# Kernel tuning notes

Measured on AMD Instinct MI355X. Metric: run time of the kernel, lower is better.

The kernel has to match this reference:

```python
import jax, jax.numpy as jnp
import numpy as np

N_NODES = 50000
N_EDGES = 150000
NODE_F, EDGE_F = 4, 11
HID, HID_OUT = 512, 1024
VS, AS_, N_ACT = 2048, 2048, 1000


def _graph_conv(x, W, b, src, dst, n, edge_weight=None):
    # DGL GraphConv, norm='both': D_out^{-1/2} on src feats, sum-aggregate, D_in^{-1/2} on dst.
    deg_out = jnp.maximum(jnp.zeros((n,), x.dtype).at[src].add(1.0), 1.0)
    deg_in = jnp.maximum(jnp.zeros((n,), x.dtype).at[dst].add(1.0), 1.0)
    h = x * (deg_out[:, None] ** -0.5)
    mult_first = W.shape[0] > W.shape[1]
    if mult_first:
        h = h @ W
    m = h[src]  # [E, d] gather
    if edge_weight is not None:
        m = m * edge_weight  # elementwise u_mul_e
    agg = jax.ops.segment_sum(m, dst, num_segments=n)
    if not mult_first:
        agg = agg @ W
    return agg * (deg_in[:, None] ** -0.5) + b


def setup_inputs() -> dict:
    key = jax.random.key(0)
    ks = jax.random.split(key, 16)
    s = 0.05
    return {
        'node_feats': jax.random.normal(ks[0], (N_NODES, NODE_F), jnp.float32),
        'edge_feats': jax.random.normal(ks[1], (N_EDGES, EDGE_F), jnp.float32),
        'W1': jax.random.normal(ks[2], (NODE_F, EDGE_F), jnp.float32) * s,
        'b1': jnp.zeros((EDGE_F,), jnp.float32),
        'W2': jax.random.normal(ks[3], (EDGE_F, HID), jnp.float32) * s,
        'b2': jnp.zeros((HID,), jnp.float32),
        'W3': jax.random.normal(ks[4], (HID, HID_OUT), jnp.float32) * s,
        'b3': jnp.zeros((HID_OUT,), jnp.float32),
        'Wv1': jax.random.normal(ks[5], (HID_OUT, VS), jnp.float32) * s,
        'bv1': jnp.zeros((VS,), jnp.float32),
        'Wv2': jax.random.normal(ks[6], (VS, 1), jnp.float32) * s,
        'bv2': jnp.zeros((1,), jnp.float32),
        'Wa1': jax.random.normal(ks[7], (HID_OUT, AS_), jnp.float32) * s,
        'ba1': jnp.zeros((AS_,), jnp.float32),
        'Wa2': jax.random.normal(ks[8], (AS_, N_ACT), jnp.float32) * s,
        'ba2': jnp.zeros((N_ACT,), jnp.float32),
        'src': jax.random.randint(ks[9], (N_EDGES,), 0, N_NODES, jnp.int32),
        'dst': jax.random.randint(ks[10], (N_EDGES,), 0, N_NODES, jnp.int32),
    }


def reference(node_feats, edge_feats, W1, b1, W2, b2, W3, b3,
              Wv1, bv1, Wv2, bv2, Wa1, ba1, Wa2, ba2, src, dst):
    n = node_feats.shape[0]
    loop = jnp.arange(n, dtype=src.dtype)
    srcL = jnp.concatenate([src, loop])  # add_self_loop
    dstL = jnp.concatenate([dst, loop])
    # self-loop edges get zero edge features (DGL default)
    ef = jnp.concatenate([edge_feats, jnp.zeros((n, edge_feats.shape[1]), edge_feats.dtype)], axis=0)

    h = jax.nn.relu(_graph_conv(node_feats, W1, b1, srcL, dstL, n))          # [N, 11]
    h = jax.nn.relu(_graph_conv(h, W2, b2, srcL, dstL, n, edge_weight=ef))   # [N, 512]
    h = _graph_conv(h, W3, b3, srcL, dstL, n)                                # [N, 1024]

    g_emb = jnp.mean(h, axis=0, keepdims=True)  # dgl.mean_nodes, single graph -> [1, 1024]

    v = jax.nn.relu(g_emb @ Wv1 + bv1) @ Wv2 + bv2        # [1, 1]
    a = jax.nn.relu(g_emb @ Wa1 + ba1) @ Wa2 + ba2        # [1, N_ACT]
    return v + (a - a.mean())
```

## Files before the change

### kernel.cpp

```cpp
#include <hip/hip_runtime.h>

#define NN 50000
#define NE 150000
#define NB 196

__global__ __launch_bounds__(256) void k_deg(const int* __restrict__ src,
                                             const int* __restrict__ dst,
                                             int* __restrict__ deg_out,
                                             int* __restrict__ deg_in) {
    int e = blockIdx.x * 256 + threadIdx.x;
    if (e < NE) {
        atomicAdd(&deg_out[src[e]], 1);
        atomicAdd(&deg_in[dst[e]], 1);
    }
}

__global__ __launch_bounds__(256) void k_bsum(const int* __restrict__ deg_in,
                                              const int* __restrict__ deg_out,
                                              int* __restrict__ bsum_in,
                                              int* __restrict__ bsum_out) {
    __shared__ int si[256], so[256];
    int t = threadIdx.x;
    int idx = blockIdx.x * 256 + t;
    si[t] = (idx < NN) ? deg_in[idx] : 0;
    so[t] = (idx < NN) ? deg_out[idx] : 0;
    __syncthreads();
    for (int off = 128; off >= 1; off >>= 1) {
        if (t < off) { si[t] += si[t + off]; so[t] += so[t + off]; }
        __syncthreads();
    }
    if (t == 0) { bsum_in[blockIdx.x] = si[0]; bsum_out[blockIdx.x] = so[0]; }
}

__global__ __launch_bounds__(256) void k_rowptr(const int* __restrict__ deg_in,
                                                const int* __restrict__ deg_out,
                                                const int* __restrict__ bsum_in,
                                                const int* __restrict__ bsum_out,
                                                const float* __restrict__ x,
                                                int* __restrict__ rp_in,
                                                int* __restrict__ rp_out,
                                                float* __restrict__ dins,
                                                float* __restrict__ douts,
                                                float4* __restrict__ xs4) {
    __shared__ int si[256], so[256];
    int b = blockIdx.x, t = threadIdx.x;
    si[t] = (t < b) ? bsum_in[t] : 0;
    so[t] = (t < b) ? bsum_out[t] : 0;
    __syncthreads();
    for (int off = 128; off >= 1; off >>= 1) {
        if (t < off) { si[t] += si[t + off]; so[t] += so[t + off]; }
        __syncthreads();
    }
    int off_in = si[0], off_out = so[0];
    __syncthreads();
    int idx = b * 256 + t;
    int di = (idx < NN) ? deg_in[idx] : 0;
    int dq = (idx < NN) ? deg_out[idx] : 0;
    si[t] = di; so[t] = dq;
    __syncthreads();
    for (int off = 1; off < 256; off <<= 1) {
        int a = (t >= off) ? si[t - off] : 0;
        int c2 = (t >= off) ? so[t - off] : 0;
        __syncthreads();
        si[t] += a; so[t] += c2;
        __syncthreads();
    }
    if (idx < NN) {
        rp_in[idx]  = off_in  + si[t] - di;
        rp_out[idx] = off_out + so[t] - dq;
        float dif = rsqrtf((float)(di + 1));
        float dqf = rsqrtf((float)(dq + 1));
        dins[idx] = dif;
        douts[idx] = dqf;
        float4 x4 = ((const float4*)x)[idx];
        x4.x *= dqf; x4.y *= dqf; x4.z *= dqf; x4.w *= dqf;
        xs4[idx] = x4;
    }
    if (b == 0 && t == 0) { rp_in[NN] = NE; rp_out[NN] = NE; }
}

__global__ __launch_bounds__(256) void k_scatter(const int* __restrict__ src,
                                                 const int* __restrict__ dst,
                                                 const float* __restrict__ ef,
                                                 const int* __restrict__ rp_in,
                                                 const int* __restrict__ rp_out,
                                                 int* __restrict__ cur_in,
                                                 int* __restrict__ cur_out,
                                                 int* __restrict__ nbr_in,
                                                 float4* __restrict__ ef4,
                                                 int* __restrict__ nbr_out) {
    int e = blockIdx.x * 256 + threadIdx.x;
    if (e >= NE) return;
    int s = src[e], d = dst[e];
    int pi = rp_in[d] + atomicAdd(&cur_in[d], 1);
    nbr_in[pi] = s;
    const float* er = ef + (size_t)e * 11;
    ef4[(size_t)pi * 3 + 0] = make_float4(er[0], er[1], er[2], er[3]);
    ef4[(size_t)pi * 3 + 1] = make_float4(er[4], er[5], er[6], er[7]);
    ef4[(size_t)pi * 3 + 2] = make_float4(er[8], er[9], er[10], 0.f);
    int po = rp_out[s] + atomicAdd(&cur_out[s], 1);
    nbr_out[po] = d;
}

__global__ __launch_bounds__(256) void k_conv1g(const float4* __restrict__ xs4,
                                                const int* __restrict__ nbr_in,
                                                const int* __restrict__ rp_in,
                                                const int* __restrict__ nbr_out,
                                                const int* __restrict__ rp_out,
                                                const float* __restrict__ dins,
                                                const float* __restrict__ douts,
                                                const float* __restrict__ W1,
                                                const float* __restrict__ b1,
                                                float4* __restrict__ h1s4,
                                                float* __restrict__ c) {
    int n = blockIdx.x * 256 + threadIdx.x;
    if (n >= NN) return;
    float din  = dins[n];
    float dout = douts[n];
    float4 a = xs4[n];
    int beg = rp_in[n], end = rp_in[n + 1];
    for (int p = beg; p < end; p++) {
        float4 xs = xs4[nbr_in[p]];
        a.x += xs.x; a.y += xs.y; a.z += xs.z; a.w += xs.w;
    }
    float cacc = din;
    int ob = rp_out[n], oe = rp_out[n + 1];
    for (int p = ob; p < oe; p++)
        cacc += dins[nbr_out[p]];
    c[n] = cacc;
    float y[12];
    #pragma unroll
    for (int j = 0; j < 11; j++) {
        float t2 = a.x * W1[0 * 11 + j] + a.y * W1[1 * 11 + j] +
                   a.z * W1[2 * 11 + j] + a.w * W1[3 * 11 + j];
        y[j] = fmaxf(fmaf(t2, din, b1[j]), 0.f) * dout;
    }
    y[11] = 0.f;
    h1s4[(size_t)n * 3 + 0] = make_float4(y[0], y[1], y[2],  y[3]);
    h1s4[(size_t)n * 3 + 1] = make_float4(y[4], y[5], y[6],  y[7]);
    h1s4[(size_t)n * 3 + 2] = make_float4(y[8], y[9], y[10], y[11]);
}

#define G2 64
__global__ __launch_bounds__(512) void k_conv2f(const float4* __restrict__ h1s4,
                                                const float4* __restrict__ ef4,
                                                const int* __restrict__ nbr_in,
                                                const int* __restrict__ rp_in,
                                                const float* __restrict__ c,
                                                const float* __restrict__ dins,
                                                const float* __restrict__ douts,
                                                const float* __restrict__ W2,
                                                const float* __restrict__ b2,
                                                float* __restrict__ t) {
    __shared__ float tile[G2 * 12];
    __shared__ int rp_sh[G2 + 1];
    __shared__ float din_sh[G2], w_sh[G2];
    int tid = threadIdx.x;
    int n0 = blockIdx.x * G2;
    if (tid <= G2) {
        int n = n0 + tid;
        rp_sh[tid] = rp_in[(n > NN) ? NN : n];
    }
    for (int i = tid; i < G2 * 12; i += 512) tile[i] = 0.f;
    if (tid < G2) {
        int n = n0 + tid;
        if (n < NN) { din_sh[tid] = dins[n]; w_sh[tid] = c[n] * douts[n] * (1.0f / NN); }
        else        { din_sh[tid] = 0.f;     w_sh[tid] = 0.f; }
    }
    __syncthreads();
    int pbeg = rp_sh[0], pend = rp_sh[G2];
    for (int p = pbeg + tid; p < pend; p += 512) {
        int s = nbr_in[p];
        float4 ha = h1s4[(size_t)s * 3 + 0];
        float4 hb = h1s4[(size_t)s * 3 + 1];
        float4 hc = h1s4[(size_t)s * 3 + 2];
        float4 ea = ef4[(size_t)p * 3 + 0];
        float4 eb = ef4[(size_t)p * 3 + 1];
        float4 ec = ef4[(size_t)p * 3 + 2];
        int lo = 0, hi = G2;
        while (hi - lo > 1) { int mid = (lo + hi) >> 1; if (rp_sh[mid] <= p) lo = mid; else hi = mid; }
        float* row = &tile[lo * 12];
        atomicAdd(&row[0],  ha.x * ea.x);
        atomicAdd(&row[1],  ha.y * ea.y);
        atomicAdd(&row[2],  ha.z * ea.z);
        atomicAdd(&row[3],  ha.w * ea.w);
        atomicAdd(&row[4],  hb.x * eb.x);
        atomicAdd(&row[5],  hb.y * eb.y);
        atomicAdd(&row[6],  hb.z * eb.z);
        atomicAdd(&row[7],  hb.w * eb.w);
        atomicAdd(&row[8],  hc.x * ec.x);
        atomicAdd(&row[9],  hc.y * ec.y);
        atomicAdd(&row[10], hc.z * ec.z);
    }
    __syncthreads();
    float w[11];
    #pragma unroll
    for (int j = 0; j < 11; j++) w[j] = W2[j * 512 + tid];
    float bias = b2[tid];
    float acc = 0.f;
    for (int i = 0; i < G2; i++) {
        const float4* trow = (const float4*)&tile[i * 12];
        float4 ta = trow[0], tb = trow[1], tc = trow[2];
        float dot = ta.x * w[0] + ta.y * w[1] + ta.z * w[2] + ta.w * w[3] +
                    tb.x * w[4] + tb.y * w[5] + tb.z * w[6] + tb.w * w[7] +
                    tc.x * w[8] + tc.y * w[9] + tc.z * w[10];
        float y = fmaxf(fmaf(dot, din_sh[i], bias), 0.f);
        acc = fmaf(w_sh[i], y, acc);
    }
    atomicAdd(&t[tid], acc);
}

__global__ __launch_bounds__(256) void k_g(const float* __restrict__ t,
                                           const float* __restrict__ W3,
                                           const float* __restrict__ b3,
                                           float* __restrict__ g) {
    int b = blockIdx.x;
    int oc = b & 3, kc = b >> 2;
    int o = oc * 256 + threadIdx.x;
    int k0 = kc * 16;
    __shared__ float ts[16];
    if (threadIdx.x < 16) ts[threadIdx.x] = t[k0 + threadIdx.x];
    __syncthreads();
    float acc = (kc == 0) ? b3[o] : 0.f;
    #pragma unroll
    for (int k = 0; k < 16; k++) acc = fmaf(ts[k], W3[(size_t)(k0 + k) * 1024 + o], acc);
    atomicAdd(&g[o], acc);
}

__global__ __launch_bounds__(256) void k_heads1(const float* __restrict__ g,
                                                const float* __restrict__ Wv1,
                                                const float* __restrict__ Wa1,
                                                float* __restrict__ hv_raw,
                                                float* __restrict__ ha_raw) {
    int b = blockIdx.x;
    int oc = b >> 5, kc = b & 31;
    int idx = oc * 256 + threadIdx.x;
    int k0 = kc * 32;
    __shared__ float gs[32];
    if (threadIdx.x < 32) gs[threadIdx.x] = g[k0 + threadIdx.x];
    __syncthreads();
    const float* W; float* outp; int o;
    if (idx < 2048) { W = Wv1; outp = hv_raw; o = idx; }
    else            { W = Wa1; outp = ha_raw; o = idx - 2048; }
    float acc = 0.f;
    #pragma unroll 8
    for (int k = 0; k < 32; k++) acc = fmaf(gs[k], W[(size_t)(k0 + k) * 2048 + o], acc);
    atomicAdd(&outp[o], acc);
}

__global__ __launch_bounds__(256) void k_heads2(const float* __restrict__ hv_raw,
                                                const float* __restrict__ bv1,
                                                const float* __restrict__ ha_raw,
                                                const float* __restrict__ ba1,
                                                const float* __restrict__ Wv2,
                                                const float* __restrict__ bv2,
                                                const float* __restrict__ Wa2,
                                                float* __restrict__ a_acc,
                                                float* __restrict__ v) {
    int b = blockIdx.x;
    int tid = threadIdx.x;
    if (b < 256) {
        int oc = b >> 6, kc = b & 63;
        int k0 = kc * 32;
        __shared__ float hs[32];
        if (tid < 32) hs[tid] = fmaxf(ha_raw[k0 + tid] + ba1[k0 + tid], 0.f);
        __syncthreads();
        int o = oc * 256 + tid;
        if (o < 1000) {
            float acc = 0.f;
            #pragma unroll 8
            for (int k = 0; k < 32; k++)
                acc = fmaf(hs[k], Wa2[(size_t)(k0 + k) * 1000 + o], acc);
            atomicAdd(&a_acc[o], acc);
        }
    } else {
        __shared__ float red[256];
        float acc = 0.f;
        for (int k = tid; k < 2048; k += 256)
            acc = fmaf(fmaxf(hv_raw[k] + bv1[k], 0.f), Wv2[k], acc);
        red[tid] = acc;
        __syncthreads();
        for (int s = 128; s >= 1; s >>= 1) {
            if (tid < s) red[tid] += red[tid + s];
            __syncthreads();
        }
        if (tid == 0) *v = red[0] + bv2[0];
    }
}

__global__ __launch_bounds__(1024) void k_final(const float* __restrict__ a_acc,
                                                const float* __restrict__ ba2,
                                                const float* __restrict__ vptr,
                                                float* __restrict__ out) {
    __shared__ float red[1024];
    int tid = threadIdx.x;
    float ai = (tid < 1000) ? a_acc[tid] + ba2[tid] : 0.f;
    red[tid] = ai;
    __syncthreads();
    for (int s = 512; s >= 1; s >>= 1) {
        if (tid < s) red[tid] += red[tid + s];
        __syncthreads();
    }
    float amean = red[0] * (1.0f / 1000.0f);
    if (tid < 1000) out[tid] = vptr[0] + ai - amean;
}

extern "C" void kernel_launch(void* const* d_in, const int* in_sizes, int n_in,
                              void* d_out, int out_size, void* d_ws, size_t ws_size,
                              hipStream_t stream) {
    const float* x   = (const float*)d_in[0];
    const float* ef  = (const float*)d_in[1];
    const float* W1  = (const float*)d_in[2];
    const float* b1  = (const float*)d_in[3];
    const float* W2  = (const float*)d_in[4];
    const float* b2  = (const float*)d_in[5];
    const float* W3  = (const float*)d_in[6];
    const float* b3  = (const float*)d_in[7];
    const float* Wv1 = (const float*)d_in[8];
    const float* bv1 = (const float*)d_in[9];
    const float* Wv2 = (const float*)d_in[10];
    const float* bv2 = (const float*)d_in[11];
    const float* Wa1 = (const float*)d_in[12];
    const float* ba1 = (const float*)d_in[13];
    const float* Wa2 = (const float*)d_in[14];
    const float* ba2 = (const float*)d_in[15];
    const int*   src = (const int*)d_in[16];
    const int*   dst = (const int*)d_in[17];
    float* out = (float*)d_out;

    char* ws = (char*)d_ws;
    size_t off = 0;
    auto alloc = [&](size_t bytes) -> void* {
        void* p = ws + off;
        off = (off + bytes + 255) & ~(size_t)255;
        return p;
    };
    int*   deg_out = (int*)  alloc(NN * 4);
    int*   deg_in  = (int*)  alloc(NN * 4);
    int*   cur_in  = (int*)  alloc(NN * 4);
    int*   cur_out = (int*)  alloc(NN * 4);
    float* t       = (float*)alloc(512 * 4);
    float* g       = (float*)alloc(1024 * 4);
    float* hv_raw  = (float*)alloc(2048 * 4);
    float* ha_raw  = (float*)alloc(2048 * 4);
    float* a_acc   = (float*)alloc(1024 * 4);
    size_t zero_bytes = off;
    int*    bsum_in  = (int*)   alloc(NB * 4);
    int*    bsum_out = (int*)   alloc(NB * 4);
    int*    rp_in    = (int*)   alloc((NN + 1) * 4);
    int*    rp_out   = (int*)   alloc((NN + 1) * 4);
    float*  dins     = (float*) alloc(NN * 4);
    float*  douts    = (float*) alloc(NN * 4);
    float4* xs4      = (float4*)alloc((size_t)NN * 16);
    int*    nbr_in   = (int*)   alloc((size_t)NE * 4);
    int*    nbr_out  = (int*)   alloc((size_t)NE * 4);
    float4* ef4      = (float4*)alloc((size_t)NE * 48);
    float4* h1s4     = (float4*)alloc((size_t)NN * 48);
    float*  c        = (float*) alloc(NN * 4);
    float*  v        = (float*) alloc(256);

    hipMemsetAsync(d_ws, 0, zero_bytes, stream);

    k_deg<<<(NE + 255) / 256, 256, 0, stream>>>(src, dst, deg_out, deg_in);
    k_bsum<<<NB, 256, 0, stream>>>(deg_in, deg_out, bsum_in, bsum_out);
    k_rowptr<<<NB, 256, 0, stream>>>(deg_in, deg_out, bsum_in, bsum_out, x,
                                     rp_in, rp_out, dins, douts, xs4);
    k_scatter<<<(NE + 255) / 256, 256, 0, stream>>>(src, dst, ef, rp_in, rp_out,
                                                    cur_in, cur_out, nbr_in, ef4, nbr_out);
    k_conv1g<<<(NN + 255) / 256, 256, 0, stream>>>(xs4, nbr_in, rp_in, nbr_out, rp_out,
                                                   dins, douts, W1, b1, h1s4, c);
    k_conv2f<<<(NN + G2 - 1) / G2, 512, 0, stream>>>(h1s4, ef4, nbr_in, rp_in, c,
                                                     dins, douts, W2, b2, t);
    k_g<<<128, 256, 0, stream>>>(t, W3, b3, g);
    k_heads1<<<512, 256, 0, stream>>>(g, Wv1, Wa1, hv_raw, ha_raw);
    k_heads2<<<257, 256, 0, stream>>>(hv_raw, bv1, ha_raw, ba1, Wv2, bv2, Wa2, a_acc, v);
    k_final<<<1, 1024, 0, stream>>>(a_acc, ba2, v, out);
}
```

Measured before the change: 210.4 us.

## Drop out-CSR, atomically accumulate c, pack dst into CSR, pad atomics

Removes the outgoing-edge CSR (rp_out, nbr_out, cur_out and its scan), so the column weight c is built in the scatter kernel by float atomics of dins[dst] onto src nodes. The in-CSR now stores (src,dst) pairs, which lets conv2 find the destination row directly instead of binary-searching the row pointers. conv2 switches to 256 threads handling two channels each over 98-node groups. Global accumulators for t, g, the head activations and a are spaced 16 floats apart to spread atomic contention across cache lines. The trade-offs are nondeterministic float atomics for c and more scattered reads in the tail kernels.

```diff
diff --git a/kernel.cpp b/kernel.cpp
--- a/kernel.cpp
+++ b/kernel.cpp
@@ -16,103 +16,89 @@
 }
 
 __global__ __launch_bounds__(256) void k_bsum(const int* __restrict__ deg_in,
-                                              const int* __restrict__ deg_out,
-                                              int* __restrict__ bsum_in,
-                                              int* __restrict__ bsum_out) {
-    __shared__ int si[256], so[256];
+                                              int* __restrict__ bsum_in) {
+    __shared__ int si[256];
     int t = threadIdx.x;
     int idx = blockIdx.x * 256 + t;
     si[t] = (idx < NN) ? deg_in[idx] : 0;
-    so[t] = (idx < NN) ? deg_out[idx] : 0;
     __syncthreads();
     for (int off = 128; off >= 1; off >>= 1) {
-        if (t < off) { si[t] += si[t + off]; so[t] += so[t + off]; }
-        __syncthreads();
-    }
-    if (t == 0) { bsum_in[blockIdx.x] = si[0]; bsum_out[blockIdx.x] = so[0]; }
+        if (t < off) si[t] += si[t + off];
+        __syncthreads();
+    }
+    if (t == 0) bsum_in[blockIdx.x] = si[0];
 }
 
 __global__ __launch_bounds__(256) void k_rowptr(const int* __restrict__ deg_in,
                                                 const int* __restrict__ deg_out,
                                                 const int* __restrict__ bsum_in,
-                                                const int* __restrict__ bsum_out,
                                                 const float* __restrict__ x,
                                                 int* __restrict__ rp_in,
-                                                int* __restrict__ rp_out,
                                                 float* __restrict__ dins,
                                                 float* __restrict__ douts,
                                                 float4* __restrict__ xs4) {
-    __shared__ int si[256], so[256];
+    __shared__ int si[256];
     int b = blockIdx.x, t = threadIdx.x;
     si[t] = (t < b) ? bsum_in[t] : 0;
-    so[t] = (t < b) ? bsum_out[t] : 0;
     __syncthreads();
     for (int off = 128; off >= 1; off >>= 1) {
-        if (t < off) { si[t] += si[t + off]; so[t] += so[t + off]; }
-        __syncthreads();
-    }
-    int off_in = si[0], off_out = so[0];
+        if (t < off) si[t] += si[t + off];
+        __syncthreads();
+    }
+    int off_in = si[0];
     __syncthreads();
     int idx = b * 256 + t;
     int di = (idx < NN) ? deg_in[idx] : 0;
-    int dq = (idx < NN) ? deg_out[idx] : 0;
-    si[t] = di; so[t] = dq;
+    si[t] = di;
     __syncthreads();
     for (int off = 1; off < 256; off <<= 1) {
         int a = (t >= off) ? si[t - off] : 0;
-        int c2 = (t >= off) ? so[t - off] : 0;
-        __syncthreads();
-        si[t] += a; so[t] += c2;
+        __syncthreads();
+        si[t] += a;
         __syncthreads();
     }
     if (idx < NN) {
-        rp_in[idx]  = off_in  + si[t] - di;
-        rp_out[idx] = off_out + so[t] - dq;
+        rp_in[idx] = off_in + si[t] - di;
         float dif = rsqrtf((float)(di + 1));
-        float dqf = rsqrtf((float)(dq + 1));
+        float dqf = rsqrtf((float)(deg_out[idx] + 1));
         dins[idx] = dif;
         douts[idx] = dqf;
         float4 x4 = ((const float4*)x)[idx];
         x4.x *= dqf; x4.y *= dqf; x4.z *= dqf; x4.w *= dqf;
         xs4[idx] = x4;
     }
-    if (b == 0 && t == 0) { rp_in[NN] = NE; rp_out[NN] = NE; }
+    if (b == 0 && t == 0) rp_in[NN] = NE;
 }
 
 __global__ __launch_bounds__(256) void k_scatter(const int* __restrict__ src,
                                                  const int* __restrict__ dst,
                                                  const float* __restrict__ ef,
                                                  const int* __restrict__ rp_in,
-                                                 const int* __restrict__ rp_out,
+                                                 const float* __restrict__ dins,
                                                  int* __restrict__ cur_in,
-                                                 int* __restrict__ cur_out,
-                                                 int* __restrict__ nbr_in,
+                                                 int2* __restrict__ ndcsr,
                                                  float4* __restrict__ ef4,
-                                                 int* __restrict__ nbr_out) {
+                                                 float* __restrict__ c) {
     int e = blockIdx.x * 256 + threadIdx.x;
     if (e >= NE) return;
     int s = src[e], d = dst[e];
     int pi = rp_in[d] + atomicAdd(&cur_in[d], 1);
-    nbr_in[pi] = s;
+    ndcsr[pi] = make_int2(s, d);
     const float* er = ef + (size_t)e * 11;
     ef4[(size_t)pi * 3 + 0] = make_float4(er[0], er[1], er[2], er[3]);
     ef4[(size_t)pi * 3 + 1] = make_float4(er[4], er[5], er[6], er[7]);
     ef4[(size_t)pi * 3 + 2] = make_float4(er[8], er[9], er[10], 0.f);
-    int po = rp_out[s] + atomicAdd(&cur_out[s], 1);
-    nbr_out[po] = d;
+    atomicAdd(&c[s], dins[d]);
 }
 
 __global__ __launch_bounds__(256) void k_conv1g(const float4* __restrict__ xs4,
-                                                const int* __restrict__ nbr_in,
+                                                const int2* __restrict__ ndcsr,
                                                 const int* __restrict__ rp_in,
-                                                const int* __restrict__ nbr_out,
-                                                const int* __restrict__ rp_out,
                                                 const float* __restrict__ dins,
                                                 const float* __restrict__ douts,
                                                 const float* __restrict__ W1,
                                                 const float* __restrict__ b1,
-                                                float4* __restrict__ h1s4,
-                                                float* __restrict__ c) {
+                                                float4* __restrict__ h1s4) {
     int n = blockIdx.x * 256 + threadIdx.x;
     if (n >= NN) return;
     float din  = dins[n];
@@ -120,14 +106,9 @@
     float4 a = xs4[n];
     int beg = rp_in[n], end = rp_in[n + 1];
     for (int p = beg; p < end; p++) {
-        float4 xs = xs4[nbr_in[p]];
+        float4 xs = xs4[ndcsr[p].x];
         a.x += xs.x; a.y += xs.y; a.z += xs.z; a.w += xs.w;
     }
-    float cacc = din;
-    int ob = rp_out[n], oe = rp_out[n + 1];
-    for (int p = ob; p < oe; p++)
-        cacc += dins[nbr_out[p]];
-    c[n] = cacc;
     float y[12];
     #pragma unroll
     for (int j = 0; j < 11; j++) {
@@ -141,45 +122,42 @@
     h1s4[(size_t)n * 3 + 2] = make_float4(y[8], y[9], y[10], y[11]);
 }
 
-#define G2 64
-__global__ __launch_bounds__(512) void k_conv2f(const float4* __restrict__ h1s4,
+#define G2 98
+__global__ __launch_bounds__(256) void k_conv2f(const float4* __restrict__ h1s4,
                                                 const float4* __restrict__ ef4,
-                                                const int* __restrict__ nbr_in,
+                                                const int2* __restrict__ ndcsr,
                                                 const int* __restrict__ rp_in,
                                                 const float* __restrict__ c,
                                                 const float* __restrict__ dins,
                                                 const float* __restrict__ douts,
                                                 const float* __restrict__ W2,
                                                 const float* __restrict__ b2,
-                                                float* __restrict__ t) {
+                                                float* __restrict__ t_pad) {
     __shared__ float tile[G2 * 12];
-    __shared__ int rp_sh[G2 + 1];
     __shared__ float din_sh[G2], w_sh[G2];
     int tid = threadIdx.x;
     int n0 = blockIdx.x * G2;
-    if (tid <= G2) {
-        int n = n0 + tid;
-        rp_sh[tid] = rp_in[(n > NN) ? NN : n];
-    }
-    for (int i = tid; i < G2 * 12; i += 512) tile[i] = 0.f;
+    int nend = (n0 + G2 < NN) ? n0 + G2 : NN;
+    for (int i = tid; i < G2 * 12; i += 256) tile[i] = 0.f;
     if (tid < G2) {
         int n = n0 + tid;
-        if (n < NN) { din_sh[tid] = dins[n]; w_sh[tid] = c[n] * douts[n] * (1.0f / NN); }
-        else        { din_sh[tid] = 0.f;     w_sh[tid] = 0.f; }
-    }
-    __syncthreads();
-    int pbeg = rp_sh[0], pend = rp_sh[G2];
-    for (int p = pbeg + tid; p < pend; p += 512) {
-        int s = nbr_in[p];
-        float4 ha = h1s4[(size_t)s * 3 + 0];
-        float4 hb = h1s4[(size_t)s * 3 + 1];
-        float4 hc = h1s4[(size_t)s * 3 + 2];
+        if (n < NN) {
+            float din = dins[n];
+            din_sh[tid] = din;
+            w_sh[tid]   = (c[n] + din) * douts[n] * (1.0f / NN);
+        } else { din_sh[tid] = 0.f; w_sh[tid] = 0.f; }
+    }
+    __syncthreads();
+    int pbeg = rp_in[n0], pend = rp_in[nend];
+    for (int p = pbeg + tid; p < pend; p += 256) {
+        int2 sd = ndcsr[p];
+        float4 ha = h1s4[(size_t)sd.x * 3 + 0];
+        float4 hb = h1s4[(size_t)sd.x * 3 + 1];
+        float4 hc = h1s4[(size_t)sd.x * 3 + 2];
         float4 ea = ef4[(size_t)p * 3 + 0];
         float4 eb = ef4[(size_t)p * 3 + 1];
         float4 ec = ef4[(size_t)p * 3 + 2];
-        int lo = 0, hi = G2;
-        while (hi - lo > 1) { int mid = (lo + hi) >> 1; if (rp_sh[mid] <= p) lo = mid; else hi = mid; }
-        float* row = &tile[lo * 12];
+        float* row = &tile[(sd.y - n0) * 12];
         atomicAdd(&row[0],  ha.x * ea.x);
         atomicAdd(&row[1],  ha.y * ea.y);
         atomicAdd(&row[2],  ha.z * ea.z);
@@ -193,69 +171,76 @@
         atomicAdd(&row[10], hc.z * ec.z);
     }
     __syncthreads();
-    float w[11];
+    int ch0 = tid, ch1 = tid + 256;
+    float w0[11], w1[11];
     #pragma unroll
-    for (int j = 0; j < 11; j++) w[j] = W2[j * 512 + tid];
-    float bias = b2[tid];
-    float acc = 0.f;
-    for (int i = 0; i < G2; i++) {
+    for (int j = 0; j < 11; j++) { w0[j] = W2[j * 512 + ch0]; w1[j] = W2[j * 512 + ch1]; }
+    float b0 = b2[ch0], b1v = b2[ch1];
+    float acc0 = 0.f, acc1 = 0.f;
+    int cnt = nend - n0;
+    for (int i = 0; i < cnt; i++) {
         const float4* trow = (const float4*)&tile[i * 12];
         float4 ta = trow[0], tb = trow[1], tc = trow[2];
-        float dot = ta.x * w[0] + ta.y * w[1] + ta.z * w[2] + ta.w * w[3] +
-                    tb.x * w[4] + tb.y * w[5] + tb.z * w[6] + tb.w * w[7] +
-                    tc.x * w[8] + tc.y * w[9] + tc.z * w[10];
-        float y = fmaxf(fmaf(dot, din_sh[i], bias), 0.f);
-        acc = fmaf(w_sh[i], y, acc);
-    }
-    atomicAdd(&t[tid], acc);
-}
-
-__global__ __launch_bounds__(256) void k_g(const float* __restrict__ t,
+        float din = din_sh[i], wn = w_sh[i];
+        float dot0 = ta.x * w0[0] + ta.y * w0[1] + ta.z * w0[2] + ta.w * w0[3] +
+                     tb.x * w0[4] + tb.y * w0[5] + tb.z * w0[6] + tb.w * w0[7] +
+                     tc.x * w0[8] + tc.y * w0[9] + tc.z * w0[10];
+        float dot1 = ta.x * w1[0] + ta.y * w1[1] + ta.z * w1[2] + ta.w * w1[3] +
+                     tb.x * w1[4] + tb.y * w1[5] + tb.z * w1[6] + tb.w * w1[7] +
+                     tc.x * w1[8] + tc.y * w1[9] + tc.z * w1[10];
+        acc0 = fmaf(wn, fmaxf(fmaf(dot0, din, b0),  0.f), acc0);
+        acc1 = fmaf(wn, fmaxf(fmaf(dot1, din, b1v), 0.f), acc1);
+    }
+    atomicAdd(&t_pad[ch0 * 16], acc0);
+    atomicAdd(&t_pad[ch1 * 16], acc1);
+}
+
+__global__ __launch_bounds__(256) void k_g(const float* __restrict__ t_pad,
                                            const float* __restrict__ W3,
                                            const float* __restrict__ b3,
-                                           float* __restrict__ g) {
+                                           float* __restrict__ g_pad) {
     int b = blockIdx.x;
     int oc = b & 3, kc = b >> 2;
     int o = oc * 256 + threadIdx.x;
     int k0 = kc * 16;
     __shared__ float ts[16];
-    if (threadIdx.x < 16) ts[threadIdx.x] = t[k0 + threadIdx.x];
+    if (threadIdx.x < 16) ts[threadIdx.x] = t_pad[(k0 + threadIdx.x) * 16];
     __syncthreads();
     float acc = (kc == 0) ? b3[o] : 0.f;
     #pragma unroll
     for (int k = 0; k < 16; k++) acc = fmaf(ts[k], W3[(size_t)(k0 + k) * 1024 + o], acc);
-    atomicAdd(&g[o], acc);
-}
-
-__global__ __launch_bounds__(256) void k_heads1(const float* __restrict__ g,
+    atomicAdd(&g_pad[o * 16], acc);
+}
+
+__global__ __launch_bounds__(256) void k_heads1(const float* __restrict__ g_pad,
                                                 const float* __restrict__ Wv1,
                                                 const float* __restrict__ Wa1,
-                                                float* __restrict__ hv_raw,
-                                                float* __restrict__ ha_raw) {
+                                                float* __restrict__ hv_pad,
+                                                float* __restrict__ ha_pad) {
     int b = blockIdx.x;
     int oc = b >> 5, kc = b & 31;
     int idx = oc * 256 + threadIdx.x;
     int k0 = kc * 32;
     __shared__ float gs[32];
-    if (threadIdx.x < 32) gs[threadIdx.x] = g[k0 + threadIdx.x];
+    if (threadIdx.x < 32) gs[threadIdx.x] = g_pad[(k0 + threadIdx.x) * 16];
     __syncthreads();
     const float* W; float* outp; int o;
-    if (idx < 2048) { W = Wv1; outp = hv_raw; o = idx; }
-    else            { W = Wa1; outp = ha_raw; o = idx - 2048; }
+    if (idx < 2048) { W = Wv1; outp = hv_pad; o = idx; }
+    else            { W = Wa1; outp = ha_pad; o = idx - 2048; }
     float acc = 0.f;
     #pragma unroll 8
     for (int k = 0; k < 32; k++) acc = fmaf(gs[k], W[(size_t)(k0 + k) * 2048 + o], acc);
-    atomicAdd(&outp[o], acc);
-}
-
-__global__ __launch_bounds__(256) void k_heads2(const float* __restrict__ hv_raw,
+    atomicAdd(&outp[o * 16], acc);
+}
+
+__global__ __launch_bounds__(256) void k_heads2(const float* __restrict__ hv_pad,
                                                 const float* __restrict__ bv1,
-                                                const float* __restrict__ ha_raw,
+                                                const float* __restrict__ ha_pad,
                                                 const float* __restrict__ ba1,
                                                 const float* __restrict__ Wv2,
                                                 const float* __restrict__ bv2,
                                                 const float* __restrict__ Wa2,
-                                                float* __restrict__ a_acc,
+                                                float* __restrict__ a_pad,
                                                 float* __restrict__ v) {
     int b = blockIdx.x;
     int tid = threadIdx.x;
@@ -263,7 +248,7 @@
         int oc = b >> 6, kc = b & 63;
         int k0 = kc * 32;
         __shared__ float hs[32];
-        if (tid < 32) hs[tid] = fmaxf(ha_raw[k0 + tid] + ba1[k0 + tid], 0.f);
+        if (tid < 32) hs[tid] = fmaxf(ha_pad[(k0 + tid) * 16] + ba1[k0 + tid], 0.f);
         __syncthreads();
         int o = oc * 256 + tid;
         if (o < 1000) {
@@ -271,13 +256,13 @@
             #pragma unroll 8
             for (int k = 0; k < 32; k++)
                 acc = fmaf(hs[k], Wa2[(size_t)(k0 + k) * 1000 + o], acc);
-            atomicAdd(&a_acc[o], acc);
+            atomicAdd(&a_pad[o * 16], acc);
         }
     } else {
         __shared__ float red[256];
         float acc = 0.f;
         for (int k = tid; k < 2048; k += 256)
-            acc = fmaf(fmaxf(hv_raw[k] + bv1[k], 0.f), Wv2[k], acc);
+            acc = fmaf(fmaxf(hv_pad[k * 16] + bv1[k], 0.f), Wv2[k], acc);
         red[tid] = acc;
         __syncthreads();
         for (int s = 128; s >= 1; s >>= 1) {
@@ -288,13 +273,13 @@
     }
 }
 
-__global__ __launch_bounds__(1024) void k_final(const float* __restrict__ a_acc,
+__global__ __launch_bounds__(1024) void k_final(const float* __restrict__ a_pad,
                                                 const float* __restrict__ ba2,
                                                 const float* __restrict__ vptr,
                                                 float* __restrict__ out) {
     __shared__ float red[1024];
     int tid = threadIdx.x;
-    float ai = (tid < 1000) ? a_acc[tid] + ba2[tid] : 0.f;
+    float ai = (tid < 1000) ? a_pad[tid * 16] + ba2[tid] : 0.f;
     red[tid] = ai;
     __syncthreads();
     for (int s = 512; s >= 1; s >>= 1) {
@@ -338,41 +323,36 @@
     int*   deg_out = (int*)  alloc(NN * 4);
     int*   deg_in  = (int*)  alloc(NN * 4);
     int*   cur_in  = (int*)  alloc(NN * 4);
-    int*   cur_out = (int*)  alloc(NN * 4);
-    float* t       = (float*)alloc(512 * 4);
-    float* g       = (float*)alloc(1024 * 4);
-    float* hv_raw  = (float*)alloc(2048 * 4);
-    float* ha_raw  = (float*)alloc(2048 * 4);
-    float* a_acc   = (float*)alloc(1024 * 4);
+    float* c       = (float*)alloc(NN * 4);
+    float* t_pad   = (float*)alloc(512 * 16 * 4);
+    float* g_pad   = (float*)alloc(1024 * 16 * 4);
+    float* hv_pad  = (float*)alloc(2048 * 16 * 4);
+    float* ha_pad  = (float*)alloc(2048 * 16 * 4);
+    float* a_pad   = (float*)alloc(1024 * 16 * 4);
     size_t zero_bytes = off;
     int*    bsum_in  = (int*)   alloc(NB * 4);
-    int*    bsum_out = (int*)   alloc(NB * 4);
     int*    rp_in    = (int*)   alloc((NN + 1) * 4);
-    int*    rp_out   = (int*)   alloc((NN + 1) * 4);
     float*  dins     = (float*) alloc(NN * 4);
     float*  douts    = (float*) alloc(NN * 4);
     float4* xs4      = (float4*)alloc((size_t)NN * 16);
-    int*    nbr_in   = (int*)   alloc((size_t)NE * 4);
-    int*    nbr_out  = (int*)   alloc((size_t)NE * 4);
+    int2*   ndcsr    = (int2*)  alloc((size_t)NE * 8);
     float4* ef4      = (float4*)alloc((size_t)NE * 48);
     float4* h1s4     = (float4*)alloc((size_t)NN * 48);
-    float*  c        = (float*) alloc(NN * 4);
     float*  v        = (float*) alloc(256);
 
     hipMemsetAsync(d_ws, 0, zero_bytes, stream);
 
     k_deg<<<(NE + 255) / 256, 256, 0, stream>>>(src, dst, deg_out, deg_in);
-    k_bsum<<<NB, 256, 0, stream>>>(deg_in, deg_out, bsum_in, bsum_out);
-    k_rowptr<<<NB, 256, 0, stream>>>(deg_in, deg_out, bsum_in, bsum_out, x,
-                                     rp_in, rp_out, dins, douts, xs4);
-    k_scatter<<<(NE + 255) / 256, 256, 0, stream>>>(src, dst, ef, rp_in, rp_out,
-                                                    cur_in, cur_out, nbr_in, ef4, nbr_out);
-    k_conv1g<<<(NN + 255) / 256, 256, 0, stream>>>(xs4, nbr_in, rp_in, nbr_out, rp_out,
-                                                   dins, douts, W1, b1, h1s4, c);
-    k_conv2f<<<(NN + G2 - 1) / G2, 512, 0, stream>>>(h1s4, ef4, nbr_in, rp_in, c,
-                                                     dins, douts, W2, b2, t);
-    k_g<<<128, 256, 0, stream>>>(t, W3, b3, g);
-    k_heads1<<<512, 256, 0, stream>>>(g, Wv1, Wa1, hv_raw, ha_raw);
-    k_heads2<<<257, 256, 0, stream>>>(hv_raw, bv1, ha_raw, ba1, Wv2, bv2, Wa2, a_acc, v);
-    k_final<<<1, 1024, 0, stream>>>(a_acc, ba2, v, out);
-}
+    k_bsum<<<NB, 256, 0, stream>>>(deg_in, bsum_in);
+    k_rowptr<<<NB, 256, 0, stream>>>(deg_in, deg_out, bsum_in, x, rp_in, dins, douts, xs4);
+    k_scatter<<<(NE + 255) / 256, 256, 0, stream>>>(src, dst, ef, rp_in, dins,
+                                                    cur_in, ndcsr, ef4, c);
+    k_conv1g<<<(NN + 255) / 256, 256, 0, stream>>>(xs4, ndcsr, rp_in, dins, douts,
+                                                   W1, b1, h1s4);
+    k_conv2f<<<(NN + G2 - 1) / G2, 256, 0, stream>>>(h1s4, ef4, ndcsr, rp_in, c,
+                                                     dins, douts, W2, b2, t_pad);
+    k_g<<<128, 256, 0, stream>>>(t_pad, W3, b3, g_pad);
+    k_heads1<<<512, 256, 0, stream>>>(g_pad, Wv1, Wa1, hv_pad, ha_pad);
+    k_heads2<<<257, 256, 0, stream>>>(hv_pad, bv1, ha_pad, ba1, Wv2, bv2, Wa2, a_pad, v);
+    k_final<<<1, 1024, 0, stream>>>(a_pad, ba2, v, out);
+}
```

New measurement: 209.6 us. Within noise of the previous version (-0.4%).
